# Kernel tuning notes

Measured on AMD Instinct MI355X. Metric: run time of the kernel, lower is better.

Reference implementation:

```python
import jax, jax.numpy as jnp
import numpy as np

ITERATIONS = 7


def _arnold_indices(n):
    # tf.meshgrid(range(width), range(height)) -> x[i,j]=j, y[i,j]=i (shape [H,W])
    x, y = jnp.meshgrid(jnp.arange(n), jnp.arange(n))
    new_x = (2 * x + y) % n
    new_y = (x + y) % n
    # tf.transpose(tf.stack([new_y,new_x],0)) reverses dims [2,H,W] -> [W,H,2],
    # so indices[i,j] = (new_y[j,i], new_x[j,i])
    return new_y.T, new_x.T


def setup_inputs() -> dict:
    key = jax.random.key(0)
    inputs = jax.random.normal(key, (16, 1024, 1024, 3), dtype=jnp.float32)
    return {"inputs": inputs}


def reference(inputs) -> jnp.ndarray:
    n = inputs.shape[1]  # square images: H == W
    iy, ix = _arnold_indices(n)  # same map every iteration
    for _ in range(ITERATIONS):
        # out[b,i,j,c] = inputs[b, iy[i,j], ix[i,j], c]  (gather_nd + map_fn, vectorized over batch)
        inputs = inputs[:, iy, ix, :]
    return inputs
```

## Files before the change

### kernel.cpp

```cpp
#include <hip/hip_runtime.h>


#define NDIM    1024
#define MASKN   1023
#define LPITCHF 193

__global__ __launch_bounds__(512) void arnold_cat7_kernel(
    const float* __restrict__ in, float* __restrict__ out) {
    __shared__ float lds[64 * LPITCHF];

    const int B     = blockIdx.x;
    const int xcd   = B & 7;
    const int q     = B >> 3;
    const int c0i   = q & 15;
    const int strip = ((q >> 4) << 3) | xcd;
    const int bimg  = strip >> 4;
    const int r0    = (strip & 15) << 6;
    const int c0    = c0i << 6;

    const int t  = threadIdx.x;
    const int w  = t >> 6;
    const int dr = t & 63;

    const float* __restrict__ inb = in  + (size_t)bimg * (size_t)(NDIM * NDIM * 3);
    float* __restrict__ outb      = out + (size_t)bimg * (size_t)(NDIM * NDIM * 3);

#pragma unroll
    for (int k = 0; k < 8; ++k) {
        const int c_local = w + 8 * k;
        const int c   = c0 + c_local;
        const int R   = (169 * c) & MASKN;
        const int col = (r0 + dr + 239 * c) & MASKN;
        const float* __restrict__ src = inb + (unsigned)(R * NDIM + col) * 3u;
        float* __restrict__ dst = &lds[c_local * LPITCHF + dr * 3];
        dst[0] = src[0];
        dst[1] = src[1];
        dst[2] = src[2];
    }
    __syncthreads();

#pragma unroll
    for (int k = 0; k < 8; ++k) {
        const int r_local = w + 8 * k;
        const int dc = dr;
        const int r  = r0 + r_local;
        const int i  = (169 * r) & MASKN;
        const int j  = (c0 + dc + 41 * i) & MASKN;
        const float* __restrict__ s = &lds[dc * LPITCHF + r_local * 3];
        float* __restrict__ d = outb + (unsigned)(i * NDIM + j) * 3u;
        d[0] = s[0];
        d[1] = s[1];
        d[2] = s[2];
    }
}

extern "C" void kernel_launch(void* const* d_in, const int* in_sizes, int n_in,
                              void* d_out, int out_size, void* d_ws, size_t ws_size,
                              hipStream_t stream) {
    (void)in_sizes; (void)n_in; (void)d_ws; (void)ws_size; (void)out_size;
    const float* in = (const float*)d_in[0];
    float* out      = (float*)d_out;
    dim3 grid(4096, 1, 1);
    dim3 block(512, 1, 1);
    hipLaunchKernelGGL(arnold_cat7_kernel, grid, block, 0, stream, in, out);
}
```

Baseline: 333.8 us.

## Retile to 256x16 blocks with vectorized 16-byte row-window gathers

Changes the tile from 64x64 to 256 rows by 16 columns so each source read becomes a contiguous 3 KB row window. The window is loaded as 16-byte vector loads, with a scalar fallback for windows that wrap around the row end. The goal is to cut the number of load instructions and make reads coalesce better. In exchange, the output writes now cover only 16 consecutive pixels per row, which may hurt write coalescing, and the LDS reads have a different bank-conflict pattern.

```diff
diff --git a/kernel.cpp b/kernel.cpp
--- a/kernel.cpp
+++ b/kernel.cpp
@@ -3,50 +3,69 @@
 
 #define NDIM    1024
 #define MASKN   1023
-#define LPITCHF 193
+#define ROWB    12288
+#define TR      256
+#define TC      16
+#define PITCHB  3120
+
+typedef float f4u __attribute__((ext_vector_type(4), aligned(4)));
 
 __global__ __launch_bounds__(512) void arnold_cat7_kernel(
     const float* __restrict__ in, float* __restrict__ out) {
-    __shared__ float lds[64 * LPITCHF];
+    __shared__ alignas(16) unsigned char lds[TC * PITCHB];
 
     const int B     = blockIdx.x;
     const int xcd   = B & 7;
     const int q     = B >> 3;
-    const int c0i   = q & 15;
-    const int strip = ((q >> 4) << 3) | xcd;
-    const int bimg  = strip >> 4;
-    const int r0    = (strip & 15) << 6;
-    const int c0    = c0i << 6;
+    const int c0i   = q & 63;
+    const int strip = ((q >> 6) << 3) | xcd;
+    const int bimg  = strip >> 2;
+    const int r0    = (strip & 3) << 8;
+    const int c0    = c0i << 4;
 
-    const int t  = threadIdx.x;
-    const int w  = t >> 6;
-    const int dr = t & 63;
+    const int t    = threadIdx.x;
+    const int w    = t >> 6;
+    const int lane = t & 63;
 
-    const float* __restrict__ inb = in  + (size_t)bimg * (size_t)(NDIM * NDIM * 3);
-    float* __restrict__ outb      = out + (size_t)bimg * (size_t)(NDIM * NDIM * 3);
+    const unsigned char* __restrict__ inb =
+        (const unsigned char*)in + (size_t)bimg * (size_t)(NDIM * ROWB);
+    float* __restrict__ outb = out + (size_t)bimg * (size_t)(NDIM * NDIM * 3);
 
 #pragma unroll
-    for (int k = 0; k < 8; ++k) {
-        const int c_local = w + 8 * k;
-        const int c   = c0 + c_local;
-        const int R   = (169 * c) & MASKN;
-        const int col = (r0 + dr + 239 * c) & MASKN;
-        const float* __restrict__ src = inb + (unsigned)(R * NDIM + col) * 3u;
-        float* __restrict__ dst = &lds[c_local * LPITCHF + dr * 3];
-        dst[0] = src[0];
-        dst[1] = src[1];
-        dst[2] = src[2];
+    for (int k = 0; k < 6; ++k) {
+        const int g    = w + 8 * k;
+        const int seg  = g / 3;
+        const int woff = g - 3 * seg;
+        const int c    = c0 + seg;
+        const int R    = (169 * c) & MASKN;
+        const int col0 = (r0 + 239 * c) & MASKN;
+        const unsigned wb = (unsigned)col0 * 12u + (unsigned)woff * 1024u;
+        const unsigned char* __restrict__ rowp = inb + (unsigned)R * (unsigned)ROWB;
+        unsigned char* __restrict__ dwin = &lds[seg * PITCHB + woff * 1024];
+
+        if (wb < (unsigned)ROWB && wb + 1024u > (unsigned)ROWB) {
+#pragma unroll
+            for (int qq = 0; qq < 4; ++qq) {
+                const unsigned o  = wb + (unsigned)(lane * 4 + qq * 256);
+                const unsigned oo = (o >= (unsigned)ROWB) ? o - (unsigned)ROWB : o;
+                *(float*)(dwin + lane * 4 + qq * 256) = *(const float*)(rowp + oo);
+            }
+        } else {
+            const unsigned o  = wb + (unsigned)(lane * 16);
+            const unsigned oo = (o >= (unsigned)ROWB) ? o - (unsigned)ROWB : o;
+            *(f4u*)(dwin + lane * 16) = *(const f4u*)(rowp + oo);
+        }
     }
     __syncthreads();
 
 #pragma unroll
     for (int k = 0; k < 8; ++k) {
-        const int r_local = w + 8 * k;
-        const int dc = dr;
-        const int r  = r0 + r_local;
-        const int i  = (169 * r) & MASKN;
+        const int p  = t + 512 * k;
+        const int rl = p >> 4;
+        const int dc = p & 15;
+        const int i  = (169 * (r0 + rl)) & MASKN;
         const int j  = (c0 + dc + 41 * i) & MASKN;
-        const float* __restrict__ s = &lds[dc * LPITCHF + r_local * 3];
+        const float* __restrict__ s = (const float*)&lds[dc * PITCHB + rl * 12];
         float* __restrict__ d = outb + (unsigned)(i * NDIM + j) * 3u;
         d[0] = s[0];
         d[1] = s[1];
```

After: 342.2 us. 1.03x slower.
